# Performance work log

Measured on AMD Instinct MI355X. Metric: run time of the kernel, lower is better.

## Reference

```python
import jax, jax.numpy as jnp
import numpy as np

N = 10000   # nodes
B = 32      # batch (hardcoded in source)
E = 40000   # edges per graph
H = 4       # attention heads
D = 10      # out_feats per head (hardcoded 10 in source)
T = 10      # GAT input feature size (hardcoded 10)
L = 2       # n_align_layers
NEG = 0.2   # LeakyReLU slope


def _leaky(z):
    return jnp.where(z >= 0, z, NEG * z)


def _ln(t):
    # LayerNorm((N,B,D), elementwise_affine=False): normalize over the whole tensor
    m = t.mean()
    v = ((t - m) ** 2).mean()
    return (t - m) * jax.lax.rsqrt(v + 1e-5)


def _gat(feat, fc_w, a_l, a_r, src, dst):
    # feat: (N,B,T); fc_w: (H*D,T); a_l,a_r: (H,D); src,dst: (E,)
    ft = jnp.einsum('nbf,of->nbo', feat, fc_w).reshape(N, B, H, D)
    el = jnp.einsum('nbhd,hd->nbh', ft, a_l)   # (N,B,H)
    er = jnp.einsum('nbhd,hd->nbh', ft, a_r)
    e = _leaky(el[src] + er[dst])              # (E,B,H)
    emax = jax.ops.segment_max(e, dst, num_segments=N)
    ee = jnp.exp(e - emax[dst])
    a = ee / jax.ops.segment_sum(ee, dst, num_segments=N)[dst]  # edge softmax per dst
    out = jax.ops.segment_sum(ft[src] * a[..., None], dst, num_segments=N)  # (N,B,H,D)
    return _leaky(out)  # activation = leaky_relu in source


def setup_inputs():
    key = jax.random.key(0)
    ks = iter(jax.random.split(key, 40))
    x = jax.random.normal(next(ks), (T, N, B, 3), dtype=jnp.float32)
    idx = lambda: jax.random.randint(next(ks), (E,), 0, N, dtype=jnp.int32)
    inp = {'x': x, 'ps_src': idx(), 'ps_dst': idx(), 'rl_src': idx(), 'rl_dst': idx()}
    def gat_params(name):
        inp[name + '_fc'] = jax.random.normal(next(ks), (L, H * D, T), dtype=jnp.float32) * 0.3
        inp[name + '_al'] = jax.random.normal(next(ks), (L, H, D), dtype=jnp.float32) * 0.3
        inp[name + '_ar'] = jax.random.normal(next(ks), (L, H, D), dtype=jnp.float32) * 0.3
    for nm in ('mu_p', 'sg_p', 'mu_r', 'sg_r'):
        gat_params(nm)
    inp['reg_mu_w'] = jax.random.normal(next(ks), (1, T), dtype=jnp.float32) * 0.3
    inp['reg_mu_b'] = jnp.zeros((1,), dtype=jnp.float32)
    inp['reg_sg_w'] = jax.random.normal(next(ks), (1, T), dtype=jnp.float32) * 0.3
    inp['reg_sg_b'] = jnp.zeros((1,), dtype=jnp.float32)
    return inp


def reference(x, mu_p_fc, mu_p_al, mu_p_ar, sg_p_fc, sg_p_al, sg_p_ar,
              mu_r_fc, mu_r_al, mu_r_ar, sg_r_fc, sg_r_al, sg_r_ar,
              reg_mu_w, reg_mu_b, reg_sg_w, reg_sg_b,
              ps_src, ps_dst, rl_src, rl_dst):
    # mode='align1' path of Net.forward
    h = jnp.transpose(x, (1, 2, 0, 3))[..., :3]  # (N,B,T,3)
    mu = h[..., 0]      # (N,B,T)
    sigma = h[..., 1]
    mu_r0, sg_r0 = mu, sigma
    # pseudo-graph alignment stack
    mu_p, sg_p = mu, sigma
    for i in range(L - 1):
        mu_p = _ln(_gat(mu_p, mu_p_fc[i], mu_p_al[i], mu_p_ar[i], ps_src, ps_dst).mean(-2))
        sg_p = _ln(_gat(sg_p, sg_p_fc[i], sg_p_al[i], sg_p_ar[i], ps_src, ps_dst).mean(-2))
        h_p = (mu_p + sg_p) / 2
        mu_p, sg_p = h_p, h_p
    # real-graph alignment stack
    mu_rl, sg_rl = mu, sigma
    for i in range(L - 1):
        mu_rl = _ln(_gat(mu_rl, mu_r_fc[i], mu_r_al[i], mu_r_ar[i], rl_src, rl_dst).mean(-2))
        sg_rl = _ln(_gat(sg_rl, sg_r_fc[i], sg_r_al[i], sg_r_ar[i], rl_src, rl_dst).mean(-2))
        h_rl = (mu_rl + sg_rl) / 2
        mu_rl, sg_rl = h_rl, h_rl
    mu_r = mu_r0 @ reg_mu_w.T + reg_mu_b                                        # (N,B,1)
    mu_pf = _gat(h_p, mu_p_fc[-1], mu_p_al[-1], mu_p_ar[-1], ps_src, ps_dst).mean(-2)
    mu_rf = _gat(h_rl, mu_r_fc[-1], mu_r_al[-1], mu_r_ar[-1], rl_src, rl_dst).mean(-2)
    sg_r = sg_r0 @ reg_sg_w.T + reg_sg_b
    sg_pf = _gat(h_p, sg_p_fc[-1], sg_p_al[-1], sg_p_ar[-1], ps_src, ps_dst).mean(-2)
    sg_rf = _gat(h_rl, sg_r_fc[-1], sg_r_al[-1], sg_r_ar[-1], rl_src, rl_dst).mean(-2)
    return ((mu_r + mu_pf + mu_rf) / 3, (sg_r + sg_pf + sg_rf) / 3)
```

## Files before the change

### kernel.cpp

```cpp
#include <hip/hip_runtime.h>

#define NN 10000
#define BB 32
#define EE 40000
#define HH 4
#define DD 10
#define TT 10
#define FS 12
#define NEG 0.2f

#define NB   (NN*BB)
#define NBT  (NN*BB*TT)
#define NBF  (NN*BB*FS)

__global__ void extract_kernel(const float* __restrict__ x,
                               const float* __restrict__ wmu, const float* __restrict__ bmu,
                               const float* __restrict__ wsg, const float* __restrict__ bsg,
                               float* __restrict__ mu, float* __restrict__ sg,
                               float* __restrict__ regmu, float* __restrict__ regsg) {
    int i = blockIdx.x * blockDim.x + threadIdx.x;
    if (i >= NB) return;
    int n = i / BB, b = i % BB;
    float smu = 0.f, ssg = 0.f;
    float muv[TT], sgv[TT];
#pragma unroll
    for (int t = 0; t < TT; t++) {
        size_t xi = (((size_t)t * NN + n) * BB + b) * 3;
        float m = x[xi], s = x[xi + 1];
        muv[t] = m; sgv[t] = s;
        smu += m * wmu[t];
        ssg += s * wsg[t];
    }
#pragma unroll
    for (int t = 0; t < TT; t++) {
        mu[(size_t)i * FS + t] = muv[t];
        sg[(size_t)i * FS + t] = sgv[t];
    }
    regmu[i] = smu + bmu[0];
    regsg[i] = ssg + bsg[0];
}

__global__ void deg_kernel(const int* __restrict__ dst, int* __restrict__ deg) {
    int e = blockIdx.x * blockDim.x + threadIdx.x;
    if (e < EE) atomicAdd(&deg[dst[e]], 1);
}

__global__ void scan_kernel(const int* __restrict__ deg, int* __restrict__ off) {
    __shared__ int sm[16];
    __shared__ int carry_s;
    int tid = threadIdx.x;
    int lane = tid & 63, wid = tid >> 6;
    if (tid == 0) { carry_s = 0; off[0] = 0; }
    __syncthreads();
    for (int base = 0; base < NN; base += 1024) {
        int i = base + tid;
        int v = (i < NN) ? deg[i] : 0;
        int x = v;
#pragma unroll
        for (int s = 1; s < 64; s <<= 1) {
            int t = __shfl_up(x, s, 64);
            if (lane >= s) x += t;
        }
        if (lane == 63) sm[wid] = x;
        __syncthreads();
        if (wid == 0) {
            int w = (lane < 16) ? sm[lane] : 0;
#pragma unroll
            for (int s = 1; s < 16; s <<= 1) {
                int t = __shfl_up(w, s, 64);
                if (lane >= s) w += t;
            }
            if (lane < 16) sm[lane] = w;
        }
        __syncthreads();
        int add = carry_s + ((wid > 0) ? sm[wid - 1] : 0);
        if (i < NN) off[i + 1] = add + x;
        int total = sm[15];
        __syncthreads();
        if (tid == 0) carry_s += total;
        __syncthreads();
    }
}

__global__ void fill_kernel(const int* __restrict__ src, const int* __restrict__ dst,
                            const int* __restrict__ off, int* __restrict__ cursor,
                            int* __restrict__ csr_src) {
    int e = blockIdx.x * blockDim.x + threadIdx.x;
    if (e < EE) {
        int d = dst[e];
        int p = atomicAdd(&cursor[d], 1);
        csr_src[off[d] + p] = src[e];
    }
}

__global__ void vpre_kernel(const float* __restrict__ fc0, const float* __restrict__ al0, const float* __restrict__ ar0,
                            const float* __restrict__ fc1, const float* __restrict__ al1, const float* __restrict__ ar1,
                            const float* __restrict__ fc2, const float* __restrict__ al2, const float* __restrict__ ar2,
                            const float* __restrict__ fc3, const float* __restrict__ al3, const float* __restrict__ ar3,
                            float* __restrict__ vbuf) {
    int j = threadIdx.x;
    if (j >= 320) return;
    int g = j / 40, r = j % 40;
    int h = r / 10, t = r % 10;
    int which = g & 3, layer = g >> 2;
    const float* fc; const float* al; const float* ar;
    if (which == 0)      { fc = fc0; al = al0; ar = ar0; }
    else if (which == 1) { fc = fc1; al = al1; ar = ar1; }
    else if (which == 2) { fc = fc2; al = al2; ar = ar2; }
    else                 { fc = fc3; al = al3; ar = ar3; }
    fc += layer * (HH * DD * TT);
    al += layer * (HH * DD);
    ar += layer * (HH * DD);
    float vl = 0.f, vr = 0.f;
#pragma unroll
    for (int d = 0; d < DD; d++) {
        float w = fc[(h * DD + d) * TT + t];
        vl += al[h * DD + d] * w;
        vr += ar[h * DD + d] * w;
    }
    vbuf[g * 80 + r] = vl;
    vbuf[g * 80 + 40 + r] = vr;
}

struct GatCfg {
    const float* f; const float* W; const float* v;
    const int* off; const int* csr;
    float* g; float* stats;
};
struct GatCfg4 { GatCfg c[4]; };

#define LOAD_ROW(dst, q)                                        \
    {                                                           \
        float4 _r0 = *(const float4*)(q);                       \
        float4 _r1 = *(const float4*)((q) + 4);                 \
        float2 _r2 = *(const float2*)((q) + 8);                 \
        dst[0]=_r0.x; dst[1]=_r0.y; dst[2]=_r0.z; dst[3]=_r0.w; \
        dst[4]=_r1.x; dst[5]=_r1.y; dst[6]=_r1.z; dst[7]=_r1.w; \
        dst[8]=_r2.x; dst[9]=_r2.y;                             \
    }

__device__ __forceinline__ void edge_accum(const float (&fa)[TT], bool val,
                                           const float* __restrict__ v,
                                           const float (&er)[HH],
                                           float (&den)[HH], float (&acc)[HH][TT]) {
#pragma unroll
    for (int h = 0; h < HH; h++) {
        float e = 0.f;
#pragma unroll
        for (int t = 0; t < TT; t++) e += v[h * TT + t] * fa[t];
        float z = e + er[h];
        z = (z >= 0.f) ? z : NEG * z;
        float w = val ? __expf(z) : 0.f;
        den[h] += w;
#pragma unroll
        for (int t = 0; t < TT; t++) acc[h][t] += w * fa[t];
    }
}

template <bool STATS>
__global__ void __launch_bounds__(256)
gat4_kernel(GatCfg4 cfgs) {
    const GatCfg cfg = cfgs.c[blockIdx.y];
    __shared__ __align__(16) float sW[HH * DD * 12];
    for (int kk = threadIdx.x; kk < HH * DD * TT; kk += blockDim.x) {
        int r = kk / TT, t = kk - r * TT;
        sW[r * 12 + t] = cfg.W[kk];
    }
    __syncthreads();

    const float* __restrict__ f   = cfg.f;
    const int*   __restrict__ csr = cfg.csr;
    const float* __restrict__ v   = cfg.v;

    int i = blockIdx.x * blockDim.x + threadIdx.x;
    float lsum = 0.f, lsq = 0.f;
    if (i < NB) {
        int b = i & 31;
        int n = i >> 5;
        int s0 = cfg.off[n], s1 = cfg.off[n + 1];

        float er[HH];
        {
            float fs[TT];
            LOAD_ROW(fs, f + (size_t)i * FS);
#pragma unroll
            for (int h = 0; h < HH; h++) {
                float e = 0.f;
#pragma unroll
                for (int t = 0; t < TT; t++) e += v[HH * TT + h * TT + t] * fs[t];
                er[h] = e;
            }
        }

        float acc[HH][TT];
        float den[HH];
#pragma unroll
        for (int h = 0; h < HH; h++) {
            den[h] = 0.f;
#pragma unroll
            for (int t = 0; t < TT; t++) acc[h][t] = 0.f;
        }

        for (int k = s0; k < s1; k += 4) {
            const float* q0; const float* q1; const float* q2; const float* q3;
            {
                int k0 = k,     k1 = k + 1, k2 = k + 2, k3 = k + 3;
                int s_0 = csr[(k0 < s1) ? k0 : s0];
                int s_1 = csr[(k1 < s1) ? k1 : s0];
                int s_2 = csr[(k2 < s1) ? k2 : s0];
                int s_3 = csr[(k3 < s1) ? k3 : s0];
                q0 = f + (size_t)(s_0 * BB + b) * FS;
                q1 = f + (size_t)(s_1 * BB + b) * FS;
                q2 = f + (size_t)(s_2 * BB + b) * FS;
                q3 = f + (size_t)(s_3 * BB + b) * FS;
            }
            float fr0[TT], fr1[TT], fr2[TT], fr3[TT];
            LOAD_ROW(fr0, q0);
            LOAD_ROW(fr1, q1);
            LOAD_ROW(fr2, q2);
            LOAD_ROW(fr3, q3);
            edge_accum(fr0, (k     < s1), v, er, den, acc);
            edge_accum(fr1, (k + 1 < s1), v, er, den, acc);
            edge_accum(fr2, (k + 2 < s1), v, er, den, acc);
            edge_accum(fr3, (k + 3 < s1), v, er, den, acc);
        }

        float rd[HH];
#pragma unroll
        for (int h = 0; h < HH; h++) rd[h] = (s1 > s0) ? (1.0f / den[h]) : 0.f;

        float outv[DD];
#pragma unroll
        for (int d = 0; d < DD; d++) outv[d] = 0.f;
#pragma unroll
        for (int h = 0; h < HH; h++) {
#pragma unroll
            for (int d = 0; d < DD; d++) {
                const float* wr = &sW[(h * DD + d) * 12];
                float4 w0 = *(const float4*)wr;
                float4 w1 = *(const float4*)(wr + 4);
                float2 w2 = *(const float2*)(wr + 8);
                float va = w0.x * acc[h][0] + w0.y * acc[h][1] + w0.z * acc[h][2] + w0.w * acc[h][3]
                         + w1.x * acc[h][4] + w1.y * acc[h][5] + w1.z * acc[h][6] + w1.w * acc[h][7]
                         + w2.x * acc[h][8] + w2.y * acc[h][9];
                va *= rd[h];
                va = (va >= 0.f) ? va : NEG * va;
                outv[d] += va * 0.25f;
            }
        }

        float* gp = cfg.g + (size_t)i * DD;
#pragma unroll
        for (int d = 0; d < DD; d += 2) {
            *(float2*)(gp + d) = make_float2(outv[d], outv[d + 1]);
            if (STATS) {
                lsum += outv[d] + outv[d + 1];
                lsq  += outv[d] * outv[d] + outv[d + 1] * outv[d + 1];
            }
        }
    }
    if (STATS) {
#pragma unroll
        for (int o = 32; o > 0; o >>= 1) {
            lsum += __shfl_down(lsum, o, 64);
            lsq  += __shfl_down(lsq, o, 64);
        }
        __shared__ float ss[4][2];
        int wid = threadIdx.x >> 6, lid = threadIdx.x & 63;
        if (lid == 0) { ss[wid][0] = lsum; ss[wid][1] = lsq; }
        __syncthreads();
        if (threadIdx.x == 0) {
            float a0 = 0.f, a1 = 0.f;
#pragma unroll
            for (int w = 0; w < 4; w++) { a0 += ss[w][0]; a1 += ss[w][1]; }
            atomicAdd(&cfg.stats[0], a0);
            atomicAdd(&cfg.stats[1], a1);
        }
    }
}

__global__ void lncomb_kernel(const float* __restrict__ ga, const float* __restrict__ gb,
                              const float* __restrict__ stats, float* __restrict__ h) {
    int i = blockIdx.x * blockDim.x + threadIdx.x;
    if (i >= NBT) return;
    const float M = (float)NBT;
    float ma = stats[0] / M; float va = stats[1] / M - ma * ma;
    float mb = stats[2] / M; float vb = stats[3] / M - mb * mb;
    float ra = rsqrtf(va + 1e-5f), rb = rsqrtf(vb + 1e-5f);
    int nb = i / DD, t = i - nb * DD;
    h[(size_t)nb * FS + t] = 0.5f * ((ga[i] - ma) * ra + (gb[i] - mb) * rb);
}

__global__ void outcomb_kernel(const float* __restrict__ reg, const float* __restrict__ ga,
                               const float* __restrict__ gb, float* __restrict__ out) {
    int i = blockIdx.x * blockDim.x + threadIdx.x;
    if (i >= NBT) return;
    int nb = i / DD;
    out[i] = (reg[nb] + ga[i] + gb[i]) * (1.0f / 3.0f);
}

extern "C" void kernel_launch(void* const* d_in, const int* in_sizes, int n_in,
                              void* d_out, int out_size, void* d_ws, size_t ws_size,
                              hipStream_t stream) {
    const float* x      = (const float*)d_in[0];
    const int* ps_src   = (const int*)d_in[1];
    const int* ps_dst   = (const int*)d_in[2];
    const int* rl_src   = (const int*)d_in[3];
    const int* rl_dst   = (const int*)d_in[4];
    const float* mu_p_fc = (const float*)d_in[5];
    const float* mu_p_al = (const float*)d_in[6];
    const float* mu_p_ar = (const float*)d_in[7];
    const float* sg_p_fc = (const float*)d_in[8];
    const float* sg_p_al = (const float*)d_in[9];
    const float* sg_p_ar = (const float*)d_in[10];
    const float* mu_r_fc = (const float*)d_in[11];
    const float* mu_r_al = (const float*)d_in[12];
    const float* mu_r_ar = (const float*)d_in[13];
    const float* sg_r_fc = (const float*)d_in[14];
    const float* sg_r_al = (const float*)d_in[15];
    const float* sg_r_ar = (const float*)d_in[16];
    const float* reg_mu_w = (const float*)d_in[17];
    const float* reg_mu_b = (const float*)d_in[18];
    const float* reg_sg_w = (const float*)d_in[19];
    const float* reg_sg_b = (const float*)d_in[20];

    float* out = (float*)d_out;

    float* fw = (float*)d_ws;
    float* mu    = fw;              fw += NBF;
    float* sigma = fw;              fw += NBF;
    float* hp    = fw;              fw += NBF;
    float* hrl   = fw;              fw += NBF;
    float* gA    = fw;              fw += NBT;
    float* gB    = fw;              fw += NBT;
    float* gA2   = fw;              fw += NBT;
    float* gB2   = fw;              fw += NBT;
    float* regmu = fw;              fw += NB;
    float* regsg = fw;              fw += NB;
    float* vbuf  = fw;              fw += 8 * 80;
    int* iw = (int*)fw;
    int* ps_off = iw;               iw += NN + 1;
    int* rl_off = iw;               iw += NN + 1;
    int* ps_csr = iw;               iw += EE;
    int* rl_csr = iw;               iw += EE;
    int* deg_ps = iw;               iw += NN;
    int* cur_ps = iw;               iw += NN;
    int* deg_rl = iw;               iw += NN;
    int* cur_rl = iw;               iw += NN;
    float* stats = (float*)iw;
    size_t zero_bytes = (size_t)(4 * NN) * sizeof(int) + 8 * sizeof(float);
    hipMemsetAsync(deg_ps, 0, zero_bytes, stream);

    const int TPB = 256;
    const int GRID_NB  = (NB + TPB - 1) / TPB;
    const int GRID_NBT = (NBT + TPB - 1) / TPB;
    const int GRID_E   = (EE + TPB - 1) / TPB;
    const int GRID_GAT = 1256;

    extract_kernel<<<GRID_NB, TPB, 0, stream>>>(x, reg_mu_w, reg_mu_b, reg_sg_w, reg_sg_b,
                                                mu, sigma, regmu, regsg);

    deg_kernel<<<GRID_E, TPB, 0, stream>>>(ps_dst, deg_ps);
    deg_kernel<<<GRID_E, TPB, 0, stream>>>(rl_dst, deg_rl);
    scan_kernel<<<1, 1024, 0, stream>>>(deg_ps, ps_off);
    scan_kernel<<<1, 1024, 0, stream>>>(deg_rl, rl_off);
    fill_kernel<<<GRID_E, TPB, 0, stream>>>(ps_src, ps_dst, ps_off, cur_ps, ps_csr);
    fill_kernel<<<GRID_E, TPB, 0, stream>>>(rl_src, rl_dst, rl_off, cur_rl, rl_csr);

    vpre_kernel<<<1, 320, 0, stream>>>(mu_p_fc, mu_p_al, mu_p_ar,
                                       sg_p_fc, sg_p_al, sg_p_ar,
                                       mu_r_fc, mu_r_al, mu_r_ar,
                                       sg_r_fc, sg_r_al, sg_r_ar, vbuf);

    {
        GatCfg4 c;
        c.c[0] = { mu,    mu_p_fc,       vbuf + 0 * 80, ps_off, ps_csr, gA,  stats + 0 };
        c.c[1] = { sigma, sg_p_fc,       vbuf + 1 * 80, ps_off, ps_csr, gB,  stats + 2 };
        c.c[2] = { mu,    mu_r_fc,       vbuf + 2 * 80, rl_off, rl_csr, gA2, stats + 4 };
        c.c[3] = { sigma, sg_r_fc,       vbuf + 3 * 80, rl_off, rl_csr, gB2, stats + 6 };
        dim3 grid(GRID_GAT, 4, 1);
        gat4_kernel<true><<<grid, TPB, 0, stream>>>(c);
    }
    lncomb_kernel<<<GRID_NBT, TPB, 0, stream>>>(gA, gB, stats + 0, hp);
    lncomb_kernel<<<GRID_NBT, TPB, 0, stream>>>(gA2, gB2, stats + 4, hrl);

    {
        GatCfg4 c;
        c.c[0] = { hp,  mu_p_fc + 400, vbuf + 4 * 80, ps_off, ps_csr, gA,  nullptr };
        c.c[1] = { hp,  sg_p_fc + 400, vbuf + 5 * 80, ps_off, ps_csr, gB,  nullptr };
        c.c[2] = { hrl, mu_r_fc + 400, vbuf + 6 * 80, rl_off, rl_csr, gA2, nullptr };
        c.c[3] = { hrl, sg_r_fc + 400, vbuf + 7 * 80, rl_off, rl_csr, gB2, nullptr };
        dim3 grid(GRID_GAT, 4, 1);
        gat4_kernel<false><<<grid, TPB, 0, stream>>>(c);
    }

    outcomb_kernel<<<GRID_NBT, TPB, 0, stream>>>(regmu, gA, gA2, out);
    outcomb_kernel<<<GRID_NBT, TPB, 0, stream>>>(regsg, gB, gB2, out + NBT);
}
```

Before: 425.3 us.

## Pair GAT computations sharing a graph into one kernel and batch setup launches

The mu and sigma GATs that use the same graph now run in one thread, reading the same CSR neighbor indices. In the first layer both features come from one interleaved row, and in the second layer a single feature row feeds two weight sets, so neighbor gathers are shared. The separate deg/scan/fill/lncomb/outcomb launches for the two graphs are merged into single launches using grid y. The cost is twice the accumulator registers per thread and half as many threads, which may lower occupancy, plus a shorter edge unroll (2 instead of 4).

```diff
diff --git a/kernel.cpp b/kernel.cpp
--- a/kernel.cpp
+++ b/kernel.cpp
@@ -7,16 +7,18 @@
 #define DD 10
 #define TT 10
 #define FS 12
+#define MS 24
 #define NEG 0.2f
 
 #define NB   (NN*BB)
 #define NBT  (NN*BB*TT)
 #define NBF  (NN*BB*FS)
+#define NBM  (NN*BB*MS)
 
 __global__ void extract_kernel(const float* __restrict__ x,
                                const float* __restrict__ wmu, const float* __restrict__ bmu,
                                const float* __restrict__ wsg, const float* __restrict__ bsg,
-                               float* __restrict__ mu, float* __restrict__ sg,
+                               float* __restrict__ ms,
                                float* __restrict__ regmu, float* __restrict__ regsg) {
     int i = blockIdx.x * blockDim.x + threadIdx.x;
     if (i >= NB) return;
@@ -33,19 +35,25 @@
     }
 #pragma unroll
     for (int t = 0; t < TT; t++) {
-        mu[(size_t)i * FS + t] = muv[t];
-        sg[(size_t)i * FS + t] = sgv[t];
+        ms[(size_t)i * MS + t]      = muv[t];
+        ms[(size_t)i * MS + 12 + t] = sgv[t];
     }
     regmu[i] = smu + bmu[0];
     regsg[i] = ssg + bsg[0];
 }
 
-__global__ void deg_kernel(const int* __restrict__ dst, int* __restrict__ deg) {
+__global__ void deg2_kernel(const int* __restrict__ dst0, int* __restrict__ deg0,
+                            const int* __restrict__ dst1, int* __restrict__ deg1) {
     int e = blockIdx.x * blockDim.x + threadIdx.x;
+    const int* dst = blockIdx.y ? dst1 : dst0;
+    int* deg       = blockIdx.y ? deg1 : deg0;
     if (e < EE) atomicAdd(&deg[dst[e]], 1);
 }
 
-__global__ void scan_kernel(const int* __restrict__ deg, int* __restrict__ off) {
+__global__ void scan2_kernel(const int* __restrict__ deg0, int* __restrict__ off0,
+                             const int* __restrict__ deg1, int* __restrict__ off1) {
+    const int* __restrict__ deg = blockIdx.x ? deg1 : deg0;
+    int* __restrict__ off       = blockIdx.x ? off1 : off0;
     __shared__ int sm[16];
     __shared__ int carry_s;
     int tid = threadIdx.x;
@@ -82,14 +90,22 @@
     }
 }
 
-__global__ void fill_kernel(const int* __restrict__ src, const int* __restrict__ dst,
-                            const int* __restrict__ off, int* __restrict__ cursor,
-                            int* __restrict__ csr_src) {
+__global__ void fill2_kernel(const int* __restrict__ src0, const int* __restrict__ dst0,
+                             const int* __restrict__ off0, int* __restrict__ cur0,
+                             int* __restrict__ csr0,
+                             const int* __restrict__ src1, const int* __restrict__ dst1,
+                             const int* __restrict__ off1, int* __restrict__ cur1,
+                             int* __restrict__ csr1) {
     int e = blockIdx.x * blockDim.x + threadIdx.x;
+    const int* src = blockIdx.y ? src1 : src0;
+    const int* dst = blockIdx.y ? dst1 : dst0;
+    const int* off = blockIdx.y ? off1 : off0;
+    int* cursor    = blockIdx.y ? cur1 : cur0;
+    int* csr       = blockIdx.y ? csr1 : csr0;
     if (e < EE) {
         int d = dst[e];
         int p = atomicAdd(&cursor[d], 1);
-        csr_src[off[d] + p] = src[e];
+        csr[off[d] + p] = src[e];
     }
 }
 
@@ -122,12 +138,15 @@
     vbuf[g * 80 + 40 + r] = vr;
 }
 
-struct GatCfg {
-    const float* f; const float* W; const float* v;
+struct PairCfg {
+    const float* f;
+    const float* WA; const float* WB;
+    const float* vA; const float* vB;
     const int* off; const int* csr;
-    float* g; float* stats;
+    float* gA; float* gB;
+    float* statsA; float* statsB;
 };
-struct GatCfg4 { GatCfg c[4]; };
+struct PairCfg2 { PairCfg c[2]; };
 
 #define LOAD_ROW(dst, q)                                        \
     {                                                           \
@@ -139,10 +158,10 @@
         dst[8]=_r2.x; dst[9]=_r2.y;                             \
     }
 
-__device__ __forceinline__ void edge_accum(const float (&fa)[TT], bool val,
-                                           const float* __restrict__ v,
-                                           const float (&er)[HH],
-                                           float (&den)[HH], float (&acc)[HH][TT]) {
+__device__ __forceinline__ void eacc(const float (&fa)[TT], bool val,
+                                     const float* __restrict__ v,
+                                     const float (&er)[HH],
+                                     float (&den)[HH], float (&acc)[HH][TT]) {
 #pragma unroll
     for (int h = 0; h < HH; h++) {
         float e = 0.f;
@@ -157,146 +176,179 @@
     }
 }
 
-template <bool STATS>
+template <bool DUALF, bool STATS>
 __global__ void __launch_bounds__(256)
-gat4_kernel(GatCfg4 cfgs) {
-    const GatCfg cfg = cfgs.c[blockIdx.y];
-    __shared__ __align__(16) float sW[HH * DD * 12];
+gatpair_kernel(PairCfg2 cfgs) {
+    const PairCfg cfg = cfgs.c[blockIdx.y];
+    __shared__ __align__(16) float sWA[HH * DD * 12];
+    __shared__ __align__(16) float sWB[HH * DD * 12];
     for (int kk = threadIdx.x; kk < HH * DD * TT; kk += blockDim.x) {
         int r = kk / TT, t = kk - r * TT;
-        sW[r * 12 + t] = cfg.W[kk];
+        sWA[r * 12 + t] = cfg.WA[kk];
+        sWB[r * 12 + t] = cfg.WB[kk];
     }
     __syncthreads();
 
     const float* __restrict__ f   = cfg.f;
     const int*   __restrict__ csr = cfg.csr;
-    const float* __restrict__ v   = cfg.v;
+    const float* __restrict__ vA  = cfg.vA;
+    const float* __restrict__ vB  = cfg.vB;
+    const int LDR = DUALF ? MS : FS;
 
     int i = blockIdx.x * blockDim.x + threadIdx.x;
-    float lsum = 0.f, lsq = 0.f;
+    float lsA = 0.f, lqA = 0.f, lsB = 0.f, lqB = 0.f;
     if (i < NB) {
         int b = i & 31;
         int n = i >> 5;
         int s0 = cfg.off[n], s1 = cfg.off[n + 1];
 
-        float er[HH];
+        float erA[HH], erB[HH];
         {
-            float fs[TT];
-            LOAD_ROW(fs, f + (size_t)i * FS);
+            const float* p = f + (size_t)i * LDR;
+            float fsA[TT];
+            LOAD_ROW(fsA, p);
+            float fsB[TT];
+            if (DUALF) { LOAD_ROW(fsB, p + 12); }
 #pragma unroll
             for (int h = 0; h < HH; h++) {
-                float e = 0.f;
-#pragma unroll
-                for (int t = 0; t < TT; t++) e += v[HH * TT + h * TT + t] * fs[t];
-                er[h] = e;
+                float ea = 0.f, eb = 0.f;
+#pragma unroll
+                for (int t = 0; t < TT; t++) {
+                    ea += vA[HH * TT + h * TT + t] * fsA[t];
+                    eb += vB[HH * TT + h * TT + t] * (DUALF ? fsB[t] : fsA[t]);
+                }
+                erA[h] = ea; erB[h] = eb;
             }
         }
 
-        float acc[HH][TT];
-        float den[HH];
+        float accA[HH][TT], accB[HH][TT];
+        float denA[HH], denB[HH];
 #pragma unroll
         for (int h = 0; h < HH; h++) {
-            den[h] = 0.f;
-#pragma unroll
-            for (int t = 0; t < TT; t++) acc[h][t] = 0.f;
-        }
-
-        for (int k = s0; k < s1; k += 4) {
-            const float* q0; const float* q1; const float* q2; const float* q3;
-            {
-                int k0 = k,     k1 = k + 1, k2 = k + 2, k3 = k + 3;
-                int s_0 = csr[(k0 < s1) ? k0 : s0];
-                int s_1 = csr[(k1 < s1) ? k1 : s0];
-                int s_2 = csr[(k2 < s1) ? k2 : s0];
-                int s_3 = csr[(k3 < s1) ? k3 : s0];
-                q0 = f + (size_t)(s_0 * BB + b) * FS;
-                q1 = f + (size_t)(s_1 * BB + b) * FS;
-                q2 = f + (size_t)(s_2 * BB + b) * FS;
-                q3 = f + (size_t)(s_3 * BB + b) * FS;
+            denA[h] = 0.f; denB[h] = 0.f;
+#pragma unroll
+            for (int t = 0; t < TT; t++) { accA[h][t] = 0.f; accB[h][t] = 0.f; }
+        }
+
+        for (int k = s0; k < s1; k += 2) {
+            int k1 = (k + 1 < s1) ? k + 1 : k;
+            bool v1 = (k + 1 < s1);
+            int e0 = csr[k], e1 = csr[k1];
+            const float* q0 = f + (size_t)(e0 * BB + b) * LDR;
+            const float* q1 = f + (size_t)(e1 * BB + b) * LDR;
+            float a0[TT], a1[TT];
+            LOAD_ROW(a0, q0);
+            LOAD_ROW(a1, q1);
+            if (DUALF) {
+                float b0[TT], b1[TT];
+                LOAD_ROW(b0, q0 + 12);
+                LOAD_ROW(b1, q1 + 12);
+                eacc(a0, true, vA, erA, denA, accA);
+                eacc(b0, true, vB, erB, denB, accB);
+                eacc(a1, v1,   vA, erA, denA, accA);
+                eacc(b1, v1,   vB, erB, denB, accB);
+            } else {
+                eacc(a0, true, vA, erA, denA, accA);
+                eacc(a0, true, vB, erB, denB, accB);
+                eacc(a1, v1,   vA, erA, denA, accA);
+                eacc(a1, v1,   vB, erB, denB, accB);
             }
-            float fr0[TT], fr1[TT], fr2[TT], fr3[TT];
-            LOAD_ROW(fr0, q0);
-            LOAD_ROW(fr1, q1);
-            LOAD_ROW(fr2, q2);
-            LOAD_ROW(fr3, q3);
-            edge_accum(fr0, (k     < s1), v, er, den, acc);
-            edge_accum(fr1, (k + 1 < s1), v, er, den, acc);
-            edge_accum(fr2, (k + 2 < s1), v, er, den, acc);
-            edge_accum(fr3, (k + 3 < s1), v, er, den, acc);
-        }
-
-        float rd[HH];
-#pragma unroll
-        for (int h = 0; h < HH; h++) rd[h] = (s1 > s0) ? (1.0f / den[h]) : 0.f;
-
-        float outv[DD];
-#pragma unroll
-        for (int d = 0; d < DD; d++) outv[d] = 0.f;
-#pragma unroll
-        for (int h = 0; h < HH; h++) {
-#pragma unroll
-            for (int d = 0; d < DD; d++) {
-                const float* wr = &sW[(h * DD + d) * 12];
-                float4 w0 = *(const float4*)wr;
-                float4 w1 = *(const float4*)(wr + 4);
-                float2 w2 = *(const float2*)(wr + 8);
-                float va = w0.x * acc[h][0] + w0.y * acc[h][1] + w0.z * acc[h][2] + w0.w * acc[h][3]
-                         + w1.x * acc[h][4] + w1.y * acc[h][5] + w1.z * acc[h][6] + w1.w * acc[h][7]
-                         + w2.x * acc[h][8] + w2.y * acc[h][9];
-                va *= rd[h];
-                va = (va >= 0.f) ? va : NEG * va;
-                outv[d] += va * 0.25f;
+        }
+
+        bool nz = (s1 > s0);
+        float* gpA = cfg.gA + (size_t)i * DD;
+        float* gpB = cfg.gB + (size_t)i * DD;
+
+#pragma unroll
+        for (int g = 0; g < 2; g++) {
+            const float (*acc)[TT] = g ? accB : accA;
+            const float* den = g ? denB : denA;
+            const float* sW  = g ? sWB : sWA;
+            float* gp        = g ? gpB : gpA;
+            float rd[HH];
+#pragma unroll
+            for (int h = 0; h < HH; h++) rd[h] = nz ? (1.0f / den[h]) : 0.f;
+            float outv[DD];
+#pragma unroll
+            for (int d = 0; d < DD; d++) outv[d] = 0.f;
+#pragma unroll
+            for (int h = 0; h < HH; h++) {
+#pragma unroll
+                for (int d = 0; d < DD; d++) {
+                    const float* wr = &sW[(h * DD + d) * 12];
+                    float4 w0 = *(const float4*)wr;
+                    float4 w1 = *(const float4*)(wr + 4);
+                    float2 w2 = *(const float2*)(wr + 8);
+                    float va = w0.x * acc[h][0] + w0.y * acc[h][1] + w0.z * acc[h][2] + w0.w * acc[h][3]
+                             + w1.x * acc[h][4] + w1.y * acc[h][5] + w1.z * acc[h][6] + w1.w * acc[h][7]
+                             + w2.x * acc[h][8] + w2.y * acc[h][9];
+                    va *= rd[h];
+                    va = (va >= 0.f) ? va : NEG * va;
+                    outv[d] += va * 0.25f;
+                }
             }
-        }
-
-        float* gp = cfg.g + (size_t)i * DD;
-#pragma unroll
-        for (int d = 0; d < DD; d += 2) {
-            *(float2*)(gp + d) = make_float2(outv[d], outv[d + 1]);
+#pragma unroll
+            for (int d = 0; d < DD; d += 2)
+                *(float2*)(gp + d) = make_float2(outv[d], outv[d + 1]);
             if (STATS) {
-                lsum += outv[d] + outv[d + 1];
-                lsq  += outv[d] * outv[d] + outv[d + 1] * outv[d + 1];
+                float s = 0.f, q = 0.f;
+#pragma unroll
+                for (int d = 0; d < DD; d++) { s += outv[d]; q += outv[d] * outv[d]; }
+                if (g) { lsB = s; lqB = q; } else { lsA = s; lqA = q; }
             }
         }
     }
     if (STATS) {
 #pragma unroll
         for (int o = 32; o > 0; o >>= 1) {
-            lsum += __shfl_down(lsum, o, 64);
-            lsq  += __shfl_down(lsq, o, 64);
-        }
-        __shared__ float ss[4][2];
+            lsA += __shfl_down(lsA, o, 64);
+            lqA += __shfl_down(lqA, o, 64);
+            lsB += __shfl_down(lsB, o, 64);
+            lqB += __shfl_down(lqB, o, 64);
+        }
+        __shared__ float ss[4][4];
         int wid = threadIdx.x >> 6, lid = threadIdx.x & 63;
-        if (lid == 0) { ss[wid][0] = lsum; ss[wid][1] = lsq; }
+        if (lid == 0) { ss[wid][0] = lsA; ss[wid][1] = lqA; ss[wid][2] = lsB; ss[wid][3] = lqB; }
         __syncthreads();
         if (threadIdx.x == 0) {
-            float a0 = 0.f, a1 = 0.f;
-#pragma unroll
-            for (int w = 0; w < 4; w++) { a0 += ss[w][0]; a1 += ss[w][1]; }
-            atomicAdd(&cfg.stats[0], a0);
-            atomicAdd(&cfg.stats[1], a1);
-        }
-    }
-}
-
-__global__ void lncomb_kernel(const float* __restrict__ ga, const float* __restrict__ gb,
-                              const float* __restrict__ stats, float* __restrict__ h) {
+            float a0 = 0.f, a1 = 0.f, a2 = 0.f, a3 = 0.f;
+#pragma unroll
+            for (int w = 0; w < 4; w++) { a0 += ss[w][0]; a1 += ss[w][1]; a2 += ss[w][2]; a3 += ss[w][3]; }
+            atomicAdd(&cfg.statsA[0], a0);
+            atomicAdd(&cfg.statsA[1], a1);
+            atomicAdd(&cfg.statsB[0], a2);
+            atomicAdd(&cfg.statsB[1], a3);
+        }
+    }
+}
+
+__global__ void lncomb2_kernel(const float* __restrict__ gA, const float* __restrict__ gB,
+                               const float* __restrict__ gA2, const float* __restrict__ gB2,
+                               const float* __restrict__ stats,
+                               float* __restrict__ hp, float* __restrict__ hrl) {
     int i = blockIdx.x * blockDim.x + threadIdx.x;
     if (i >= NBT) return;
+    const float* ga = blockIdx.y ? gA2 : gA;
+    const float* gb = blockIdx.y ? gB2 : gB;
+    const float* st = stats + (blockIdx.y ? 4 : 0);
+    float* h        = blockIdx.y ? hrl : hp;
     const float M = (float)NBT;
-    float ma = stats[0] / M; float va = stats[1] / M - ma * ma;
-    float mb = stats[2] / M; float vb = stats[3] / M - mb * mb;
+    float ma = st[0] / M; float va = st[1] / M - ma * ma;
+    float mb = st[2] / M; float vb = st[3] / M - mb * mb;
     float ra = rsqrtf(va + 1e-5f), rb = rsqrtf(vb + 1e-5f);
     int nb = i / DD, t = i - nb * DD;
     h[(size_t)nb * FS + t] = 0.5f * ((ga[i] - ma) * ra + (gb[i] - mb) * rb);
 }
 
-__global__ void outcomb_kernel(const float* __restrict__ reg, const float* __restrict__ ga,
-                               const float* __restrict__ gb, float* __restrict__ out) {
+__global__ void outcomb2_kernel(const float* __restrict__ regmu, const float* __restrict__ regsg,
+                                const float* __restrict__ gA, const float* __restrict__ gA2,
+                                const float* __restrict__ gB, const float* __restrict__ gB2,
+                                float* __restrict__ out) {
     int i = blockIdx.x * blockDim.x + threadIdx.x;
     if (i >= NBT) return;
     int nb = i / DD;
-    out[i] = (reg[nb] + ga[i] + gb[i]) * (1.0f / 3.0f);
+    if (blockIdx.y == 0) out[i]       = (regmu[nb] + gA[i] + gA2[i]) * (1.0f / 3.0f);
+    else                 out[NBT + i] = (regsg[nb] + gB[i] + gB2[i]) * (1.0f / 3.0f);
 }
 
 extern "C" void kernel_launch(void* const* d_in, const int* in_sizes, int n_in,
@@ -327,8 +379,7 @@
     float* out = (float*)d_out;
 
     float* fw = (float*)d_ws;
-    float* mu    = fw;              fw += NBF;
-    float* sigma = fw;              fw += NBF;
+    float* ms    = fw;              fw += NBM;
     float* hp    = fw;              fw += NBF;
     float* hrl   = fw;              fw += NBF;
     float* gA    = fw;              fw += NBT;
@@ -355,17 +406,17 @@
     const int GRID_NB  = (NB + TPB - 1) / TPB;
     const int GRID_NBT = (NBT + TPB - 1) / TPB;
     const int GRID_E   = (EE + TPB - 1) / TPB;
-    const int GRID_GAT = 1256;
 
     extract_kernel<<<GRID_NB, TPB, 0, stream>>>(x, reg_mu_w, reg_mu_b, reg_sg_w, reg_sg_b,
-                                                mu, sigma, regmu, regsg);
-
-    deg_kernel<<<GRID_E, TPB, 0, stream>>>(ps_dst, deg_ps);
-    deg_kernel<<<GRID_E, TPB, 0, stream>>>(rl_dst, deg_rl);
-    scan_kernel<<<1, 1024, 0, stream>>>(deg_ps, ps_off);
-    scan_kernel<<<1, 1024, 0, stream>>>(deg_rl, rl_off);
-    fill_kernel<<<GRID_E, TPB, 0, stream>>>(ps_src, ps_dst, ps_off, cur_ps, ps_csr);
-    fill_kernel<<<GRID_E, TPB, 0, stream>>>(rl_src, rl_dst, rl_off, cur_rl, rl_csr);
+                                                ms, regmu, regsg);
+
+    {
+        dim3 g(GRID_E, 2, 1);
+        deg2_kernel<<<g, TPB, 0, stream>>>(ps_dst, deg_ps, rl_dst, deg_rl);
+        scan2_kernel<<<2, 1024, 0, stream>>>(deg_ps, ps_off, deg_rl, rl_off);
+        fill2_kernel<<<g, TPB, 0, stream>>>(ps_src, ps_dst, ps_off, cur_ps, ps_csr,
+                                            rl_src, rl_dst, rl_off, cur_rl, rl_csr);
+    }
 
     vpre_kernel<<<1, 320, 0, stream>>>(mu_p_fc, mu_p_al, mu_p_ar,
                                        sg_p_fc, sg_p_al, sg_p_ar,
@@ -373,27 +424,31 @@
                                        sg_r_fc, sg_r_al, sg_r_ar, vbuf);
 
     {
-        GatCfg4 c;
-        c.c[0] = { mu,    mu_p_fc,       vbuf + 0 * 80, ps_off, ps_csr, gA,  stats + 0 };
-        c.c[1] = { sigma, sg_p_fc,       vbuf + 1 * 80, ps_off, ps_csr, gB,  stats + 2 };
-        c.c[2] = { mu,    mu_r_fc,       vbuf + 2 * 80, rl_off, rl_csr, gA2, stats + 4 };
-        c.c[3] = { sigma, sg_r_fc,       vbuf + 3 * 80, rl_off, rl_csr, gB2, stats + 6 };
-        dim3 grid(GRID_GAT, 4, 1);
-        gat4_kernel<true><<<grid, TPB, 0, stream>>>(c);
-    }
-    lncomb_kernel<<<GRID_NBT, TPB, 0, stream>>>(gA, gB, stats + 0, hp);
-    lncomb_kernel<<<GRID_NBT, TPB, 0, stream>>>(gA2, gB2, stats + 4, hrl);
-
+        PairCfg2 c;
+        c.c[0] = { ms, mu_p_fc, sg_p_fc, vbuf + 0 * 80, vbuf + 1 * 80,
+                   ps_off, ps_csr, gA,  gB,  stats + 0, stats + 2 };
+        c.c[1] = { ms, mu_r_fc, sg_r_fc, vbuf + 2 * 80, vbuf + 3 * 80,
+                   rl_off, rl_csr, gA2, gB2, stats + 4, stats + 6 };
+        dim3 grid(GRID_NB, 2, 1);
+        gatpair_kernel<true, true><<<grid, TPB, 0, stream>>>(c);
+    }
     {
-        GatCfg4 c;
-        c.c[0] = { hp,  mu_p_fc + 400, vbuf + 4 * 80, ps_off, ps_csr, gA,  nullptr };
-        c.c[1] = { hp,  sg_p_fc + 400, vbuf + 5 * 80, ps_off, ps_csr, gB,  nullptr };
-        c.c[2] = { hrl, mu_r_fc + 400, vbuf + 6 * 80, rl_off, rl_csr, gA2, nullptr };
-        c.c[3] = { hrl, sg_r_fc + 400, vbuf + 7 * 80, rl_off, rl_csr, gB2, nullptr };
-        dim3 grid(GRID_GAT, 4, 1);
-        gat4_kernel<false><<<grid, TPB, 0, stream>>>(c);
-    }
-
-    outcomb_kernel<<<GRID_NBT, TPB, 0, stream>>>(regmu, gA, gA2, out);
-    outcomb_kernel<<<GRID_NBT, TPB, 0, stream>>>(regsg, gB, gB2, out + NBT);
-}
+        dim3 g(GRID_NBT, 2, 1);
+        lncomb2_kernel<<<g, TPB, 0, stream>>>(gA, gB, gA2, gB2, stats, hp, hrl);
+    }
+
+    {
+        PairCfg2 c;
+        c.c[0] = { hp,  mu_p_fc + 400, sg_p_fc + 400, vbuf + 4 * 80, vbuf + 5 * 80,
+                   ps_off, ps_csr, gA,  gB,  nullptr, nullptr };
+        c.c[1] = { hrl, mu_r_fc + 400, sg_r_fc + 400, vbuf + 6 * 80, vbuf + 7 * 80,
+                   rl_off, rl_csr, gA2, gB2, nullptr, nullptr };
+        dim3 grid(GRID_NB, 2, 1);
+        gatpair_kernel<false, false><<<grid, TPB, 0, stream>>>(c);
+    }
+
+    {
+        dim3 g(GRID_NBT, 2, 1);
+        outcomb2_kernel<<<g, TPB, 0, stream>>>(regmu, regsg, gA, gA2, gB, gB2, out);
+    }
+}
```

Result: no change. 420.4 us (-1.1%).
